# Optimization experiments

Hardware: AMD Instinct MI355X
Metric: run time of the kernel (lower is better)

Reference implementation:

```python
import jax, jax.numpy as jnp
import numpy as np

B, L, D, H = 64, 24, 512, 512


def setup_inputs() -> dict:
    key = jax.random.key(0)
    ks = jax.random.split(key, 6)
    inp = jax.random.normal(ks[0], (B, L, D), jnp.float32)
    length = jax.random.randint(ks[1], (B,), L // 2, L + 1)  # valid lengths in [L/2, L]
    # word_linear: word_dim -> 2*hidden_dim (kaiming normal, zero bias)
    word_W = jax.random.normal(ks[2], (2 * H, D), jnp.float32) * (2.0 / D) ** 0.5
    word_b = jnp.zeros((2 * H,), jnp.float32)
    # comp_linear: 2*hidden_dim -> 5*hidden_dim (TreeLSTM gates i, fl, fr, u, o)
    comp_W = jax.random.normal(ks[3], (5 * H, 2 * H), jnp.float32) * (1.0 / H) ** 0.5
    comp_b = jnp.zeros((5 * H,), jnp.float32)
    comp_query = jax.random.normal(ks[4], (H,), jnp.float32) * 0.01
    return dict(inp=inp, length=length, word_W=word_W, word_b=word_b,
                comp_W=comp_W, comp_b=comp_b, comp_query=comp_query)


def _tree_lstm_forward(inp, word_W, word_b, comp_W, comp_b, comp_query, length):
    max_depth = inp.shape[1]
    length_mask = jnp.arange(max_depth)[None, :] < length[:, None]  # (B, L) bool
    # leaf states: word_linear output chunked into (h, c)
    hc = inp @ word_W.T + word_b  # (B, L, 2H)
    h, c = jnp.split(hc, 2, axis=2)
    for i in range(max_depth - 1):  # sequential merge over shrinking length
        hl, cl = h[:, :-1, :], c[:, :-1, :]
        hr, cr = h[:, 1:, :], c[:, 1:, :]
        # BinaryTreeLSTMLayer: fused gate linear on [hl; hr]
        v = jnp.concatenate([hl, hr], axis=2) @ comp_W.T + comp_b  # (B, L-i-1, 5H)
        gi, gfl, gfr, gu, go = jnp.split(v, 5, axis=2)
        new_c = (cl * jax.nn.sigmoid(gfl + 1.0)
                 + cr * jax.nn.sigmoid(gfr + 1.0)
                 + jnp.tanh(gu) * jax.nn.sigmoid(gi))
        new_h = jax.nn.sigmoid(go) * jnp.tanh(new_c)
        if i < max_depth - 2:
            # select_composition: greedy (eval-mode) one-hot over query-dot scores
            scores = jnp.einsum('blh,h->bl', new_h, comp_query)  # (B, L-i-1)
            m = length_mask[:, i + 1:]
            masked = jnp.where(m, scores, -1e9)
            sel = jax.lax.stop_gradient(
                jax.nn.one_hot(jnp.argmax(masked, axis=1), masked.shape[1], dtype=new_h.dtype))
            cum = jnp.cumsum(sel, axis=1)
            left = 1.0 - cum
            right = jnp.concatenate(
                [jnp.zeros((sel.shape[0], 1), sel.dtype), cum[:, :-1]], axis=1)
            new_h = sel[..., None] * new_h + left[..., None] * hl + right[..., None] * hr
            new_c = sel[..., None] * new_c + left[..., None] * cl + right[..., None] * cr
        # update_state: only advance rows whose sequence is still active
        done = length_mask[:, i + 1].astype(new_h.dtype)[:, None, None]
        h = done * new_h + (1.0 - done) * h[:, :-1, :]
        c = done * new_c + (1.0 - done) * c[:, :-1, :]
    return h[:, 0, :]  # (B, H) root hidden state


def reference(inp, length, word_W, word_b, comp_W, comp_b, comp_query):
    return _tree_lstm_forward(inp, word_W, word_b, comp_W, comp_b, comp_query, length)
```

## Files before the change

kernel.cpp:

```cpp
#include <hip/hip_runtime.h>
#include <math.h>

#define BB 64
#define LL 24
#define DD 512
#define GG 2560
#define NSTEP 23
#define NTILES 160

__device__ __forceinline__ float sigm(float x) { return 1.0f / (1.0f + __expf(-x)); }

__device__ __forceinline__ unsigned short f2bf(float x) {
    unsigned u = __float_as_uint(x);
    unsigned r = (u + 0x7fff + ((u >> 16) & 1)) >> 16;
    return (unsigned short)r;
}
__device__ __forceinline__ float bf2f(unsigned short b) {
    return __uint_as_float(((unsigned)b) << 16);
}

using short8 = __attribute__((ext_vector_type(8))) short;
using f32x4 = __attribute__((ext_vector_type(4))) float;

__global__ __launch_bounds__(256) void gemm_big(const float* __restrict__ A,
                                                const float* __restrict__ Wt,
                                                float* __restrict__ O0,
                                                float* __restrict__ O1) {
    __shared__ float As[16][132];
    __shared__ float Bs[16][132];
    const int tid = threadIdx.x;
    const int n0 = blockIdx.x * 128;
    const int m0 = blockIdx.y * 128;
    const int tn = tid & 15;
    const int tm = tid >> 4;

    float acc[8][8];
#pragma unroll
    for (int y = 0; y < 8; ++y)
#pragma unroll
        for (int x = 0; x < 8; ++x) acc[y][x] = 0.f;

    for (int kt = 0; kt < 512; kt += 16) {
#pragma unroll
        for (int ii = 0; ii < 2; ++ii) {
            int idx = tid + ii * 256;
            int r = idx >> 2, c4 = idx & 3;
            float4 v = *(const float4*)(A + (size_t)(m0 + r) * DD + kt + c4 * 4);
            As[c4 * 4 + 0][r] = v.x;
            As[c4 * 4 + 1][r] = v.y;
            As[c4 * 4 + 2][r] = v.z;
            As[c4 * 4 + 3][r] = v.w;
        }
#pragma unroll
        for (int ii = 0; ii < 2; ++ii) {
            int idx = tid + ii * 256;
            int r = idx >> 2, c4 = idx & 3;
            int n = n0 + r;
            const float* wrow = (n < GG) ? (Wt + (size_t)n * (2 * DD))
                                         : (Wt + (size_t)(n - GG) * (2 * DD) + DD);
            float4 v = *(const float4*)(wrow + kt + c4 * 4);
            Bs[c4 * 4 + 0][r] = v.x;
            Bs[c4 * 4 + 1][r] = v.y;
            Bs[c4 * 4 + 2][r] = v.z;
            Bs[c4 * 4 + 3][r] = v.w;
        }
        __syncthreads();
#pragma unroll
        for (int k = 0; k < 16; ++k) {
            float4 a0 = *(const float4*)&As[k][tm * 8];
            float4 a1 = *(const float4*)&As[k][tm * 8 + 4];
            float4 b0 = *(const float4*)&Bs[k][tn * 4];
            float4 b1 = *(const float4*)&Bs[k][64 + tn * 4];
            float av[8] = {a0.x, a0.y, a0.z, a0.w, a1.x, a1.y, a1.z, a1.w};
            float bv[8] = {b0.x, b0.y, b0.z, b0.w, b1.x, b1.y, b1.z, b1.w};
#pragma unroll
            for (int y = 0; y < 8; ++y)
#pragma unroll
                for (int x = 0; x < 8; ++x) acc[y][x] += av[y] * bv[x];
        }
        __syncthreads();
    }

#pragma unroll
    for (int y = 0; y < 8; ++y) {
        const int m = m0 + tm * 8 + y;
#pragma unroll
        for (int g = 0; g < 2; ++g) {
            int n = n0 + g * 64 + tn * 4;
            float4 v;
            v.x = acc[y][g * 4 + 0];
            v.y = acc[y][g * 4 + 1];
            v.z = acc[y][g * 4 + 2];
            v.w = acc[y][g * 4 + 3];
            float* dst = (n < GG) ? (O0 + (size_t)m * GG + n)
                                  : (O1 + (size_t)m * GG + (n - GG));
            *(float4*)dst = v;
        }
    }
}

__global__ __launch_bounds__(256) void gemm64w(const float* __restrict__ A,
                                               const float* __restrict__ Wt,
                                               const float* __restrict__ bias,
                                               float* __restrict__ O0,
                                               float* __restrict__ O1) {
    __shared__ float As[16][68];
    __shared__ float Bs[16][132];
    const int tid = threadIdx.x;
    const int n0 = blockIdx.x * 128;
    const int m0 = blockIdx.y * 64;
    const int tn = tid & 15;
    const int tm = tid >> 4;

    float acc[4][8];
#pragma unroll
    for (int y = 0; y < 4; ++y)
#pragma unroll
        for (int x = 0; x < 8; ++x) acc[y][x] = 0.f;

    for (int kt = 0; kt < 512; kt += 16) {
        {
            int r = tid >> 2, c4 = tid & 3;
            float4 v = *(const float4*)(A + (size_t)(m0 + r) * DD + kt + c4 * 4);
            As[c4 * 4 + 0][r] = v.x;
            As[c4 * 4 + 1][r] = v.y;
            As[c4 * 4 + 2][r] = v.z;
            As[c4 * 4 + 3][r] = v.w;
        }
#pragma unroll
        for (int ii = 0; ii < 2; ++ii) {
            int idx = tid + ii * 256;
            int r = idx >> 2, c4 = idx & 3;
            float4 v = *(const float4*)(Wt + (size_t)(n0 + r) * DD + kt + c4 * 4);
            Bs[c4 * 4 + 0][r] = v.x;
            Bs[c4 * 4 + 1][r] = v.y;
            Bs[c4 * 4 + 2][r] = v.z;
            Bs[c4 * 4 + 3][r] = v.w;
        }
        __syncthreads();
#pragma unroll
        for (int k = 0; k < 16; ++k) {
            float4 a = *(const float4*)&As[k][tm * 4];
            float4 b0 = *(const float4*)&Bs[k][tn * 4];
            float4 b1 = *(const float4*)&Bs[k][64 + tn * 4];
            float av[4] = {a.x, a.y, a.z, a.w};
            float bv[8] = {b0.x, b0.y, b0.z, b0.w, b1.x, b1.y, b1.z, b1.w};
#pragma unroll
            for (int y = 0; y < 4; ++y)
#pragma unroll
                for (int x = 0; x < 8; ++x) acc[y][x] += av[y] * bv[x];
        }
        __syncthreads();
    }

#pragma unroll
    for (int y = 0; y < 4; ++y) {
        const int m = m0 + tm * 4 + y;
#pragma unroll
        for (int g = 0; g < 2; ++g) {
            int n = n0 + g * 64 + tn * 4;
            float4 v;
            v.x = acc[y][g * 4 + 0] + bias[n + 0];
            v.y = acc[y][g * 4 + 1] + bias[n + 1];
            v.z = acc[y][g * 4 + 2] + bias[n + 2];
            v.w = acc[y][g * 4 + 3] + bias[n + 3];
            float* dst = (n < DD) ? (O0 + (size_t)m * DD + n)
                                  : (O1 + (size_t)m * DD + (n - DD));
            *(float4*)dst = v;
        }
    }
}

__global__ __launch_bounds__(256) void splitW_k(const float* __restrict__ comp_W,
                                                unsigned short* __restrict__ Wh,
                                                unsigned short* __restrict__ Wl) {
    int t = (blockIdx.x * 256 + threadIdx.x) * 4;
    int n = t >> 9;
    int k = t & 511;
    const float* src = (n < GG) ? (comp_W + (size_t)n * (2 * DD) + k)
                                : (comp_W + (size_t)(n - GG) * (2 * DD) + DD + k);
    float4 v = *(const float4*)src;
    ushort4 h, l;
    h.x = f2bf(v.x); l.x = f2bf(v.x - bf2f(h.x));
    h.y = f2bf(v.y); l.y = f2bf(v.y - bf2f(h.y));
    h.z = f2bf(v.z); l.z = f2bf(v.z - bf2f(h.z));
    h.w = f2bf(v.w); l.w = f2bf(v.w - bf2f(h.w));
    *(ushort4*)(Wh + t) = h;
    *(ushort4*)(Wl + t) = l;
}

__device__ __forceinline__ float half_dot(const float* __restrict__ ar,
                                          const float* __restrict__ br,
                                          const float* __restrict__ cb,
                                          const float* __restrict__ cl,
                                          const float* __restrict__ cr,
                                          const float* __restrict__ q, int lane) {
    float part = 0.f;
#pragma unroll
    for (int d = lane; d < DD; d += 128) {
        float gi = ar[d] + br[d] + cb[d];
        float gfl = ar[DD + d] + br[DD + d] + cb[DD + d];
        float gfr = ar[2 * DD + d] + br[2 * DD + d] + cb[2 * DD + d];
        float gu = ar[3 * DD + d] + br[3 * DD + d] + cb[3 * DD + d];
        float go = ar[4 * DD + d] + br[4 * DD + d] + cb[4 * DD + d];
        float nc = cl[d] * sigm(gfl + 1.f) + cr[d] * sigm(gfr + 1.f) + tanhf(gu) * sigm(gi);
        part += sigm(go) * tanhf(nc) * q[d];
    }
#pragma unroll
    for (int off = 32; off; off >>= 1) part += __shfl_down(part, off);
    return part;
}

__device__ __forceinline__ void gate2n(const float* __restrict__ ar,
                                       const float* __restrict__ br,
                                       const float* __restrict__ cb,
                                       const float* __restrict__ cl,
                                       const float* __restrict__ cr, int d,
                                       float nh[2], float nc[2]) {
    float2 A0 = *(const float2*)(ar + d),          B0 = *(const float2*)(br + d);
    float2 A1 = *(const float2*)(ar + DD + d),     B1 = *(const float2*)(br + DD + d);
    float2 A2 = *(const float2*)(ar + 2 * DD + d), B2 = *(const float2*)(br + 2 * DD + d);
    float2 A3 = *(const float2*)(ar + 3 * DD + d), B3 = *(const float2*)(br + 3 * DD + d);
    float2 A4 = *(const float2*)(ar + 4 * DD + d), B4 = *(const float2*)(br + 4 * DD + d);
    float2 C0 = *(const float2*)(cb + d);
    float2 C1 = *(const float2*)(cb + DD + d);
    float2 C2 = *(const float2*)(cb + 2 * DD + d);
    float2 C3 = *(const float2*)(cb + 3 * DD + d);
    float2 C4 = *(const float2*)(cb + 4 * DD + d);
    float2 CL = *(const float2*)(cl + d);
    float2 CR = *(const float2*)(cr + d);
    float gi0 = A0.x + B0.x + C0.x, gi1 = A0.y + B0.y + C0.y;
    float gfl0 = A1.x + B1.x + C1.x, gfl1 = A1.y + B1.y + C1.y;
    float gfr0 = A2.x + B2.x + C2.x, gfr1 = A2.y + B2.y + C2.y;
    float gu0 = A3.x + B3.x + C3.x, gu1 = A3.y + B3.y + C3.y;
    float go0 = A4.x + B4.x + C4.x, go1 = A4.y + B4.y + C4.y;
    nc[0] = CL.x * sigm(gfl0 + 1.f) + CR.x * sigm(gfr0 + 1.f) + tanhf(gu0) * sigm(gi0);
    nc[1] = CL.y * sigm(gfl1 + 1.f) + CR.y * sigm(gfr1 + 1.f) + tanhf(gu1) * sigm(gi1);
    nh[0] = sigm(go0) * tanhf(nc[0]);
    nh[1] = sigm(go1) * tanhf(nc[1]);
}

__global__ __launch_bounds__(256) void scoreall_k(const float* __restrict__ acache,
                                                  const float* __restrict__ bcache,
                                                  const float* __restrict__ cbuf,
                                                  const float* __restrict__ compb,
                                                  const float* __restrict__ q,
                                                  float* __restrict__ scores_g) {
    __shared__ float red_s[4];
    const int tid = threadIdx.x;
    const int b = blockIdx.y;
    const int p = blockIdx.x * 2 + (tid >> 7);
    const bool valid = p < NSTEP;
    float w = 0.f;
    if (valid) {
        w = half_dot(acache + (size_t)(b * LL + p) * GG,
                     bcache + (size_t)(b * LL + p + 1) * GG, compb,
                     cbuf + (size_t)(b * LL + p) * DD,
                     cbuf + (size_t)(b * LL + p + 1) * DD, q, tid & 127);
    }
    if ((tid & 63) == 0) red_s[tid >> 6] = w;
    __syncthreads();
    if ((tid == 0 || tid == 128) && valid) {
        int base = tid >> 6;
        scores_g[b * NSTEP + p] = red_s[base] + red_s[base + 1];
    }
}

__global__ __launch_bounds__(256) void stepA_k(
    int i, const int* __restrict__ length, float* __restrict__ cbuf,
    const float* __restrict__ acache, const float* __restrict__ bcache,
    float* __restrict__ hout, unsigned short* __restrict__ hh,
    unsigned short* __restrict__ hl, float* __restrict__ scores_g,
    int* __restrict__ seq_g, int* __restrict__ kp_g, int* __restrict__ msel,
    const float* __restrict__ compb, const float* __restrict__ q, float* __restrict__ out) {
    __shared__ float red_s[4];
    __shared__ float sc_l[32];
    __shared__ int seq_l[32];
    __shared__ int k_sh;
    const int tid = threadIdx.x;
    const int b = blockIdx.x;
    const int lane7 = tid & 127;
    const int lenb = length[b];
    const int ncand = NSTEP - i;

    if (i == 0) {
        if (tid < LL) seq_l[tid] = tid;
    } else {
        if (tid < LL - i) seq_l[tid] = seq_g[b * 32 + tid];
    }
    if (tid < ncand) sc_l[tid] = scores_g[b * NSTEP + tid];
    __syncthreads();
    const int kp = (i > 0) ? kp_g[b] : 0;

    if (i > 0 && i < lenb) {
        int p = (tid < 128) ? (kp - 1) : kp;
        bool valid = (p >= 0) && (p < ncand);
        float w = 0.f;
        if (valid) {
            int sl = seq_l[p], sr = seq_l[p + 1];
            const float* ar = acache + (size_t)(b * LL + sl) * GG;
            const float* br = bcache + (size_t)(b * LL + sr) * GG;
            const float* cl = cbuf + (size_t)(b * LL + sl) * DD;
            const float* cr = cbuf + (size_t)(b * LL + sr) * DD;
#pragma unroll
            for (int pass = 0; pass < 2; ++pass) {
                int d = pass * 256 + lane7 * 2;
                float nh[2], nc[2];
                gate2n(ar, br, compb, cl, cr, d, nh, nc);
                float2 Q = *(const float2*)(q + d);
                w += nh[0] * Q.x + nh[1] * Q.y;
            }
#pragma unroll
            for (int off = 32; off; off >>= 1) w += __shfl_down(w, off);
        }
        if ((tid & 63) == 0) red_s[tid >> 6] = w;
        __syncthreads();
        if (tid == 0) {
            if (kp - 1 >= 0) sc_l[kp - 1] = red_s[0] + red_s[1];
            if (kp < ncand) sc_l[kp] = red_s[2] + red_s[3];
        }
        __syncthreads();
    }

    if (i + 1 < lenb) {
        if (tid == 0) {
            const int vmax = lenb - i - 2;
            int k = 0;
            float best = sc_l[0];
            for (int pp = 1; pp <= vmax; ++pp)
                if (sc_l[pp] > best) { best = sc_l[pp]; k = pp; }
            k_sh = k;
        }
        __syncthreads();
        const int k = k_sh;
        const int sl = seq_l[k], sr = seq_l[k + 1];
        const float* ar = acache + (size_t)(b * LL + sl) * GG;
        const float* br = bcache + (size_t)(b * LL + sr) * GG;
        const float* cl = cbuf + (size_t)(b * LL + sl) * DD;
        const float* cr = cbuf + (size_t)(b * LL + sr) * DD;
        {
            const int d = 2 * tid;
            float nh[2], nc[2];
            gate2n(ar, br, compb, cl, cr, d, nh, nc);
            *(float2*)(cbuf + (size_t)(b * LL + sl) * DD + d) = make_float2(nc[0], nc[1]);
            *(float2*)(hout + (size_t)b * DD + d) = make_float2(nh[0], nh[1]);
            ushort2 hv, lv;
            hv.x = f2bf(nh[0]); lv.x = f2bf(nh[0] - bf2f(hv.x));
            hv.y = f2bf(nh[1]); lv.y = f2bf(nh[1] - bf2f(hv.y));
            *(ushort2*)(hh + (size_t)b * DD + d) = hv;
            *(ushort2*)(hl + (size_t)b * DD + d) = lv;
            if (i == NSTEP - 1)
                *(float2*)(out + (size_t)b * DD + d) = make_float2(nh[0], nh[1]);
        }
        float sv = (tid + 1 < ncand) ? sc_l[tid + 1] : 0.f;
        int qv = (tid + 1 < LL - i) ? seq_l[tid + 1] : 0;
        __syncthreads();
        if (tid >= k + 1 && tid <= ncand - 2) sc_l[tid] = sv;
        if (tid >= k + 1 && tid <= LL - i - 2) seq_l[tid] = qv;
        if (tid < ncand - 1) scores_g[b * NSTEP + tid] = sc_l[tid];
        if (tid < LL - i - 1) seq_g[b * 32 + tid] = seq_l[tid];
        if (tid == 0) { kp_g[b] = k; msel[b] = sl; }
    } else if (i == NSTEP - 1) {
        const int d = 2 * tid;
        *(float2*)(out + (size_t)b * DD + d) = *(const float2*)(hout + (size_t)b * DD + d);
    }
}

__global__ __launch_bounds__(256) void stepB_mfma(
    const unsigned short* __restrict__ hh, const unsigned short* __restrict__ hl,
    const int* __restrict__ msel,
    const unsigned short* __restrict__ Wh, const unsigned short* __restrict__ Wl,
    float* __restrict__ acache, float* __restrict__ bcache) {
    __shared__ int msel_s[BB];
    const int tid = threadIdx.x;
    const int bid = blockIdx.x;
    if (tid < BB) msel_s[tid] = msel[tid];
    __syncthreads();

    const int w = tid >> 6, lane = tid & 63;
    const int mt0 = (w >> 1) * 2;
    const int nt = w & 1;
    const int lr = lane & 15;
    const int kg = lane >> 4;
    const int n = bid * 32 + nt * 16 + lr;

    const unsigned short* wh_row = Wh + (size_t)n * DD;
    const unsigned short* wl_row = Wl + (size_t)n * DD;
    const unsigned short* a0h_row = hh + (size_t)(mt0 * 16 + lr) * DD;
    const unsigned short* a0l_row = hl + (size_t)(mt0 * 16 + lr) * DD;
    const unsigned short* a1h_row = a0h_row + 16 * DD;
    const unsigned short* a1l_row = a0l_row + 16 * DD;

    f32x4 acc0 = {0.f, 0.f, 0.f, 0.f};
    f32x4 acc1 = {0.f, 0.f, 0.f, 0.f};

#pragma unroll 4
    for (int ks = 0; ks < 16; ++ks) {
        const int kb = ks * 32 + kg * 8;
        short8 bh = *(const short8*)(wh_row + kb);
        short8 bl = *(const short8*)(wl_row + kb);
        short8 a0h = *(const short8*)(a0h_row + kb);
        short8 a0l = *(const short8*)(a0l_row + kb);
        short8 a1h = *(const short8*)(a1h_row + kb);
        short8 a1l = *(const short8*)(a1l_row + kb);
        acc0 = __builtin_amdgcn_mfma_f32_16x16x32_bf16(a0h, bh, acc0, 0, 0, 0);
        acc1 = __builtin_amdgcn_mfma_f32_16x16x32_bf16(a1h, bh, acc1, 0, 0, 0);
        acc0 = __builtin_amdgcn_mfma_f32_16x16x32_bf16(a0l, bh, acc0, 0, 0, 0);
        acc1 = __builtin_amdgcn_mfma_f32_16x16x32_bf16(a1l, bh, acc1, 0, 0, 0);
        acc0 = __builtin_amdgcn_mfma_f32_16x16x32_bf16(a0h, bl, acc0, 0, 0, 0);
        acc1 = __builtin_amdgcn_mfma_f32_16x16x32_bf16(a1h, bl, acc1, 0, 0, 0);
    }

#pragma unroll
    for (int t = 0; t < 2; ++t) {
        f32x4 acc = t ? acc1 : acc0;
        const int mbase = (mt0 + t) * 16 + kg * 4;
#pragma unroll
        for (int r = 0; r < 4; ++r) {
            int m = mbase + r;
            size_t row = (size_t)(m * LL + msel_s[m]);
            float* dst = (n < GG) ? (acache + row * GG + n)
                                  : (bcache + row * GG + (n - GG));
            *dst = acc[r];
        }
    }
}

extern "C" void kernel_launch(void* const* d_in, const int* in_sizes, int n_in, void* d_out,
                              int out_size, void* d_ws, size_t ws_size, hipStream_t stream) {
    const float* inp = (const float*)d_in[0];
    const int* length = (const int*)d_in[1];
    const float* word_W = (const float*)d_in[2];
    const float* word_b = (const float*)d_in[3];
    const float* comp_W = (const float*)d_in[4];
    const float* comp_b = (const float*)d_in[5];
    const float* comp_q = (const float*)d_in[6];
    float* out = (float*)d_out;

    float* ws = (float*)d_ws;
    size_t off = 0;
    float* hbuf = ws + off;   off += (size_t)BB * LL * DD;
    float* cbuf = ws + off;   off += (size_t)BB * LL * DD;
    float* acache = ws + off; off += (size_t)BB * LL * GG;
    float* bcache = ws + off; off += (size_t)BB * LL * GG;
    float* hout = ws + off;   off += (size_t)BB * DD;
    float* scores = ws + off; off += 2048;
    int* seq_g = (int*)(ws + off); off += BB * 32;
    int* kp_g = (int*)(ws + off);  off += 64;
    int* msel = (int*)(ws + off);  off += 64;
    unsigned short* Wh = (unsigned short*)(ws + off); off += (size_t)5120 * DD / 2;
    unsigned short* Wl = (unsigned short*)(ws + off); off += (size_t)5120 * DD / 2;
    unsigned short* hh = (unsigned short*)(ws + off); off += (size_t)BB * DD / 2;
    unsigned short* hl = (unsigned short*)(ws + off); off += (size_t)BB * DD / 2;
    (void)ws_size; (void)in_sizes; (void)n_in; (void)out_size;

    splitW_k<<<2560, 256, 0, stream>>>(comp_W, Wh, Wl);

    gemm64w<<<dim3(8, 24), 256, 0, stream>>>(inp, word_W, word_b, hbuf, cbuf);

    gemm_big<<<dim3(40, 12), 256, 0, stream>>>(hbuf, comp_W, acache, bcache);

    scoreall_k<<<dim3(12, 64), 256, 0, stream>>>(acache, bcache, cbuf, comp_b, comp_q, scores);

    for (int i = 0; i < NSTEP; ++i) {
        stepA_k<<<BB, 256, 0, stream>>>(i, length, cbuf, acache, bcache, hout, hh, hl,
                                        scores, seq_g, kp_g, msel, comp_b, comp_q, out);
        if (i < NSTEP - 1) {
            stepB_mfma<<<NTILES, 256, 0, stream>>>(hh, hl, msel, Wh, Wl, acache, bcache);
        }
    }
}
```

Measured before the change: 688.0 us.

## Replace FP32 leaf-gate GEMM with split-bf16 MFMA GEMM

The large precompute GEMM of leaf hidden states against both halves of comp_W now runs on MFMA bf16 instructions. It uses a three-product hi/lo split (hi*hi + hi*lo + lo*hi) to keep close to FP32 accuracy. The word-linear GEMM writes the h half directly as bf16 hi/lo pairs, which removes the FP32 hbuf and its round trip. The MFMA kernel loads operands straight from global memory without LDS staging. Its output stores are scalar and strided, which may limit store bandwidth.

Result: faster. 656.6 us (-4.6%).

```diff
diff --git a/kernel.cpp b/kernel.cpp
--- a/kernel.cpp
+++ b/kernel.cpp
@@ -21,155 +21,6 @@
 
 using short8 = __attribute__((ext_vector_type(8))) short;
 using f32x4 = __attribute__((ext_vector_type(4))) float;
-
-__global__ __launch_bounds__(256) void gemm_big(const float* __restrict__ A,
-                                                const float* __restrict__ Wt,
-                                                float* __restrict__ O0,
-                                                float* __restrict__ O1) {
-    __shared__ float As[16][132];
-    __shared__ float Bs[16][132];
-    const int tid = threadIdx.x;
-    const int n0 = blockIdx.x * 128;
-    const int m0 = blockIdx.y * 128;
-    const int tn = tid & 15;
-    const int tm = tid >> 4;
-
-    float acc[8][8];
-#pragma unroll
-    for (int y = 0; y < 8; ++y)
-#pragma unroll
-        for (int x = 0; x < 8; ++x) acc[y][x] = 0.f;
-
-    for (int kt = 0; kt < 512; kt += 16) {
-#pragma unroll
-        for (int ii = 0; ii < 2; ++ii) {
-            int idx = tid + ii * 256;
-            int r = idx >> 2, c4 = idx & 3;
-            float4 v = *(const float4*)(A + (size_t)(m0 + r) * DD + kt + c4 * 4);
-            As[c4 * 4 + 0][r] = v.x;
-            As[c4 * 4 + 1][r] = v.y;
-            As[c4 * 4 + 2][r] = v.z;
-            As[c4 * 4 + 3][r] = v.w;
-        }
-#pragma unroll
-        for (int ii = 0; ii < 2; ++ii) {
-            int idx = tid + ii * 256;
-            int r = idx >> 2, c4 = idx & 3;
-            int n = n0 + r;
-            const float* wrow = (n < GG) ? (Wt + (size_t)n * (2 * DD))
-                                         : (Wt + (size_t)(n - GG) * (2 * DD) + DD);
-            float4 v = *(const float4*)(wrow + kt + c4 * 4);
-            Bs[c4 * 4 + 0][r] = v.x;
-            Bs[c4 * 4 + 1][r] = v.y;
-            Bs[c4 * 4 + 2][r] = v.z;
-            Bs[c4 * 4 + 3][r] = v.w;
-        }
-        __syncthreads();
-#pragma unroll
-        for (int k = 0; k < 16; ++k) {
-            float4 a0 = *(const float4*)&As[k][tm * 8];
-            float4 a1 = *(const float4*)&As[k][tm * 8 + 4];
-            float4 b0 = *(const float4*)&Bs[k][tn * 4];
-            float4 b1 = *(const float4*)&Bs[k][64 + tn * 4];
-            float av[8] = {a0.x, a0.y, a0.z, a0.w, a1.x, a1.y, a1.z, a1.w};
-            float bv[8] = {b0.x, b0.y, b0.z, b0.w, b1.x, b1.y, b1.z, b1.w};
-#pragma unroll
-            for (int y = 0; y < 8; ++y)
-#pragma unroll
-                for (int x = 0; x < 8; ++x) acc[y][x] += av[y] * bv[x];
-        }
-        __syncthreads();
-    }
-
-#pragma unroll
-    for (int y = 0; y < 8; ++y) {
-        const int m = m0 + tm * 8 + y;
-#pragma unroll
-        for (int g = 0; g < 2; ++g) {
-            int n = n0 + g * 64 + tn * 4;
-            float4 v;
-            v.x = acc[y][g * 4 + 0];
-            v.y = acc[y][g * 4 + 1];
-            v.z = acc[y][g * 4 + 2];
-            v.w = acc[y][g * 4 + 3];
-            float* dst = (n < GG) ? (O0 + (size_t)m * GG + n)
-                                  : (O1 + (size_t)m * GG + (n - GG));
-            *(float4*)dst = v;
-        }
-    }
-}
-
-__global__ __launch_bounds__(256) void gemm64w(const float* __restrict__ A,
-                                               const float* __restrict__ Wt,
-                                               const float* __restrict__ bias,
-                                               float* __restrict__ O0,
-                                               float* __restrict__ O1) {
-    __shared__ float As[16][68];
-    __shared__ float Bs[16][132];
-    const int tid = threadIdx.x;
-    const int n0 = blockIdx.x * 128;
-    const int m0 = blockIdx.y * 64;
-    const int tn = tid & 15;
-    const int tm = tid >> 4;
-
-    float acc[4][8];
-#pragma unroll
-    for (int y = 0; y < 4; ++y)
-#pragma unroll
-        for (int x = 0; x < 8; ++x) acc[y][x] = 0.f;
-
-    for (int kt = 0; kt < 512; kt += 16) {
-        {
-            int r = tid >> 2, c4 = tid & 3;
-            float4 v = *(const float4*)(A + (size_t)(m0 + r) * DD + kt + c4 * 4);
-            As[c4 * 4 + 0][r] = v.x;
-            As[c4 * 4 + 1][r] = v.y;
-            As[c4 * 4 + 2][r] = v.z;
-            As[c4 * 4 + 3][r] = v.w;
-        }
-#pragma unroll
-        for (int ii = 0; ii < 2; ++ii) {
-            int idx = tid + ii * 256;
-            int r = idx >> 2, c4 = idx & 3;
-            float4 v = *(const float4*)(Wt + (size_t)(n0 + r) * DD + kt + c4 * 4);
-            Bs[c4 * 4 + 0][r] = v.x;
-            Bs[c4 * 4 + 1][r] = v.y;
-            Bs[c4 * 4 + 2][r] = v.z;
-            Bs[c4 * 4 + 3][r] = v.w;
-        }
-        __syncthreads();
-#pragma unroll
-        for (int k = 0; k < 16; ++k) {
-            float4 a = *(const float4*)&As[k][tm * 4];
-            float4 b0 = *(const float4*)&Bs[k][tn * 4];
-            float4 b1 = *(const float4*)&Bs[k][64 + tn * 4];
-            float av[4] = {a.x, a.y, a.z, a.w};
-            float bv[8] = {b0.x, b0.y, b0.z, b0.w, b1.x, b1.y, b1.z, b1.w};
-#pragma unroll
-            for (int y = 0; y < 4; ++y)
-#pragma unroll
-                for (int x = 0; x < 8; ++x) acc[y][x] += av[y] * bv[x];
-        }
-        __syncthreads();
-    }
-
-#pragma unroll
-    for (int y = 0; y < 4; ++y) {
-        const int m = m0 + tm * 4 + y;
-#pragma unroll
-        for (int g = 0; g < 2; ++g) {
-            int n = n0 + g * 64 + tn * 4;
-            float4 v;
-            v.x = acc[y][g * 4 + 0] + bias[n + 0];
-            v.y = acc[y][g * 4 + 1] + bias[n + 1];
-            v.z = acc[y][g * 4 + 2] + bias[n + 2];
-            v.w = acc[y][g * 4 + 3] + bias[n + 3];
-            float* dst = (n < DD) ? (O0 + (size_t)m * DD + n)
-                                  : (O1 + (size_t)m * DD + (n - DD));
-            *(float4*)dst = v;
-        }
-    }
-}
 
 __global__ __launch_bounds__(256) void splitW_k(const float* __restrict__ comp_W,
                                                 unsigned short* __restrict__ Wh,
@@ -187,6 +38,157 @@
     h.w = f2bf(v.w); l.w = f2bf(v.w - bf2f(h.w));
     *(ushort4*)(Wh + t) = h;
     *(ushort4*)(Wl + t) = l;
+}
+
+__global__ __launch_bounds__(256) void gemm64w(const float* __restrict__ A,
+                                               const float* __restrict__ Wt,
+                                               const float* __restrict__ bias,
+                                               unsigned short* __restrict__ Ah,
+                                               unsigned short* __restrict__ Al,
+                                               float* __restrict__ O1) {
+    __shared__ float As[16][68];
+    __shared__ float Bs[16][132];
+    const int tid = threadIdx.x;
+    const int n0 = blockIdx.x * 128;
+    const int m0 = blockIdx.y * 64;
+    const int tn = tid & 15;
+    const int tm = tid >> 4;
+
+    float acc[4][8];
+#pragma unroll
+    for (int y = 0; y < 4; ++y)
+#pragma unroll
+        for (int x = 0; x < 8; ++x) acc[y][x] = 0.f;
+
+    for (int kt = 0; kt < 512; kt += 16) {
+        {
+            int r = tid >> 2, c4 = tid & 3;
+            float4 v = *(const float4*)(A + (size_t)(m0 + r) * DD + kt + c4 * 4);
+            As[c4 * 4 + 0][r] = v.x;
+            As[c4 * 4 + 1][r] = v.y;
+            As[c4 * 4 + 2][r] = v.z;
+            As[c4 * 4 + 3][r] = v.w;
+        }
+#pragma unroll
+        for (int ii = 0; ii < 2; ++ii) {
+            int idx = tid + ii * 256;
+            int r = idx >> 2, c4 = idx & 3;
+            float4 v = *(const float4*)(Wt + (size_t)(n0 + r) * DD + kt + c4 * 4);
+            Bs[c4 * 4 + 0][r] = v.x;
+            Bs[c4 * 4 + 1][r] = v.y;
+            Bs[c4 * 4 + 2][r] = v.z;
+            Bs[c4 * 4 + 3][r] = v.w;
+        }
+        __syncthreads();
+#pragma unroll
+        for (int k = 0; k < 16; ++k) {
+            float4 a = *(const float4*)&As[k][tm * 4];
+            float4 b0 = *(const float4*)&Bs[k][tn * 4];
+            float4 b1 = *(const float4*)&Bs[k][64 + tn * 4];
+            float av[4] = {a.x, a.y, a.z, a.w};
+            float bv[8] = {b0.x, b0.y, b0.z, b0.w, b1.x, b1.y, b1.z, b1.w};
+#pragma unroll
+            for (int y = 0; y < 4; ++y)
+#pragma unroll
+                for (int x = 0; x < 8; ++x) acc[y][x] += av[y] * bv[x];
+        }
+        __syncthreads();
+    }
+
+#pragma unroll
+    for (int y = 0; y < 4; ++y) {
+        const int m = m0 + tm * 4 + y;
+#pragma unroll
+        for (int g = 0; g < 2; ++g) {
+            int n = n0 + g * 64 + tn * 4;
+            float4 v;
+            v.x = acc[y][g * 4 + 0] + bias[n + 0];
+            v.y = acc[y][g * 4 + 1] + bias[n + 1];
+            v.z = acc[y][g * 4 + 2] + bias[n + 2];
+            v.w = acc[y][g * 4 + 3] + bias[n + 3];
+            if (n < DD) {
+                ushort4 hv, lv;
+                hv.x = f2bf(v.x); lv.x = f2bf(v.x - bf2f(hv.x));
+                hv.y = f2bf(v.y); lv.y = f2bf(v.y - bf2f(hv.y));
+                hv.z = f2bf(v.z); lv.z = f2bf(v.z - bf2f(hv.z));
+                hv.w = f2bf(v.w); lv.w = f2bf(v.w - bf2f(hv.w));
+                *(ushort4*)(Ah + (size_t)m * DD + n) = hv;
+                *(ushort4*)(Al + (size_t)m * DD + n) = lv;
+            } else {
+                *(float4*)(O1 + (size_t)m * DD + (n - DD)) = v;
+            }
+        }
+    }
+}
+
+__global__ __launch_bounds__(256) void gemm_big_mfma(
+    const unsigned short* __restrict__ Ah, const unsigned short* __restrict__ Al,
+    const unsigned short* __restrict__ Wh, const unsigned short* __restrict__ Wl,
+    float* __restrict__ O0, float* __restrict__ O1) {
+    const int tid = threadIdx.x;
+    const int n0 = blockIdx.x * 128;
+    const int m0 = blockIdx.y * 128;
+    const int w = tid >> 6, lane = tid & 63;
+    const int mq = w >> 1, nq = w & 1;
+    const int lr = lane & 15, kg = lane >> 4;
+    const int kofs = kg * 8;
+
+    const unsigned short* pah[4];
+    const unsigned short* pal[4];
+    const unsigned short* pbh[4];
+    const unsigned short* pbl[4];
+#pragma unroll
+    for (int t = 0; t < 4; ++t) {
+        int mrow = m0 + mq * 64 + t * 16 + lr;
+        pah[t] = Ah + (size_t)mrow * DD + kofs;
+        pal[t] = Al + (size_t)mrow * DD + kofs;
+        int nrow = n0 + nq * 64 + t * 16 + lr;
+        pbh[t] = Wh + (size_t)nrow * DD + kofs;
+        pbl[t] = Wl + (size_t)nrow * DD + kofs;
+    }
+
+    f32x4 acc[4][4];
+#pragma unroll
+    for (int mt = 0; mt < 4; ++mt)
+#pragma unroll
+        for (int nt = 0; nt < 4; ++nt) acc[mt][nt] = (f32x4){0.f, 0.f, 0.f, 0.f};
+
+#pragma unroll 2
+    for (int ks = 0; ks < 16; ++ks) {
+        const int kb = ks * 32;
+        short8 ah[4], al[4], bh[4], bl[4];
+#pragma unroll
+        for (int t = 0; t < 4; ++t) {
+            ah[t] = *(const short8*)(pah[t] + kb);
+            al[t] = *(const short8*)(pal[t] + kb);
+            bh[t] = *(const short8*)(pbh[t] + kb);
+            bl[t] = *(const short8*)(pbl[t] + kb);
+        }
+#pragma unroll
+        for (int mt = 0; mt < 4; ++mt)
+#pragma unroll
+            for (int nt = 0; nt < 4; ++nt) {
+                acc[mt][nt] = __builtin_amdgcn_mfma_f32_16x16x32_bf16(al[mt], bh[nt], acc[mt][nt], 0, 0, 0);
+                acc[mt][nt] = __builtin_amdgcn_mfma_f32_16x16x32_bf16(ah[mt], bl[nt], acc[mt][nt], 0, 0, 0);
+                acc[mt][nt] = __builtin_amdgcn_mfma_f32_16x16x32_bf16(ah[mt], bh[nt], acc[mt][nt], 0, 0, 0);
+            }
+    }
+
+#pragma unroll
+    for (int mt = 0; mt < 4; ++mt) {
+        const int mbase = m0 + mq * 64 + mt * 16 + kg * 4;
+#pragma unroll
+        for (int nt = 0; nt < 4; ++nt) {
+            const int n = n0 + nq * 64 + nt * 16 + lr;
+#pragma unroll
+            for (int r = 0; r < 4; ++r) {
+                const int m = mbase + r;
+                float* dst = (n < GG) ? (O0 + (size_t)m * GG + n)
+                                      : (O1 + (size_t)m * GG + (n - GG));
+                *dst = acc[mt][nt][r];
+            }
+        }
+    }
 }
 
 __device__ __forceinline__ float half_dot(const float* __restrict__ ar,
@@ -439,7 +441,6 @@
 
     float* ws = (float*)d_ws;
     size_t off = 0;
-    float* hbuf = ws + off;   off += (size_t)BB * LL * DD;
     float* cbuf = ws + off;   off += (size_t)BB * LL * DD;
     float* acache = ws + off; off += (size_t)BB * LL * GG;
     float* bcache = ws + off; off += (size_t)BB * LL * GG;
@@ -452,13 +453,15 @@
     unsigned short* Wl = (unsigned short*)(ws + off); off += (size_t)5120 * DD / 2;
     unsigned short* hh = (unsigned short*)(ws + off); off += (size_t)BB * DD / 2;
     unsigned short* hl = (unsigned short*)(ws + off); off += (size_t)BB * DD / 2;
+    unsigned short* Ah = (unsigned short*)(ws + off); off += (size_t)BB * LL * DD / 2;
+    unsigned short* Al = (unsigned short*)(ws + off); off += (size_t)BB * LL * DD / 2;
     (void)ws_size; (void)in_sizes; (void)n_in; (void)out_size;
 
     splitW_k<<<2560, 256, 0, stream>>>(comp_W, Wh, Wl);
 
-    gemm64w<<<dim3(8, 24), 256, 0, stream>>>(inp, word_W, word_b, hbuf, cbuf);
-
-    gemm_big<<<dim3(40, 12), 256, 0, stream>>>(hbuf, comp_W, acache, bcache);
+    gemm64w<<<dim3(8, 24), 256, 0, stream>>>(inp, word_W, word_b, Ah, Al, cbuf);
+
+    gemm_big_mfma<<<dim3(40, 12), 256, 0, stream>>>(Ah, Al, Wh, Wl, acache, bcache);
 
     scoreall_k<<<dim3(12, 64), 256, 0, stream>>>(acache, bcache, cbuf, comp_b, comp_q, scores);
 
```
